# Performance work log

Measured on AMD Instinct MI355X. Metric: run time of the kernel, lower is better.

The kernel has to match this reference:

```python
import jax, jax.numpy as jnp
import numpy as np

B = 262144
MA = [128, 128]
MB = [128, 128]


def krone_linear(x_a, x_b, wa, wb, ba, bb):
    # slice inputs to each branch's in_features (torch slices the wider branch)
    ia, ib = wa.shape[1], wb.shape[1]
    x_a = x_a[:, :ia]
    x_b = x_b[:, :ib]
    h_a = x_a @ wa.T + ba
    h_b = x_b @ wb.T + bb
    # zero-pad the narrower output so both branches share a width (static shapes)
    oa, ob = wa.shape[0], wb.shape[0]
    if oa > ob:
        h_b = jnp.pad(h_b, ((0, 0), (0, oa - ob)))
    elif ob > oa:
        h_a = jnp.pad(h_a, ((0, 0), (0, ob - oa)))
    return h_a, h_b


def krone_softmax(x_a, x_b, fa, fb):
    x_a = x_a[:, :fa]
    x_b = x_b[:, :fb]
    # vectorized per-row Kronecker product: kron(a, b)[i*fb + j] = a[i]*b[j]
    y = (x_a[:, :, None] * x_b[:, None, :]).reshape(x_a.shape[0], fa * fb)
    return jax.nn.softmax(y, axis=1)


def setup_inputs() -> dict:
    key = jax.random.key(0)
    ks = jax.random.split(key, 13)
    s = 0.1
    inp = {
        "x": jax.random.normal(ks[0], (2, B, 2), dtype=jnp.float32),
        "w1a": jax.random.normal(ks[1], (MA[0], 2), dtype=jnp.float32) * s,
        "w1b": jax.random.normal(ks[2], (MB[0], 2), dtype=jnp.float32) * s,
        "b1a": jax.random.normal(ks[3], (MA[0],), dtype=jnp.float32) * s,
        "b1b": jax.random.normal(ks[4], (MB[0],), dtype=jnp.float32) * s,
        "w2a": jax.random.normal(ks[5], (MA[1], MA[0]), dtype=jnp.float32) * s,
        "w2b": jax.random.normal(ks[6], (MB[1], MB[0]), dtype=jnp.float32) * s,
        "b2a": jax.random.normal(ks[7], (MA[1],), dtype=jnp.float32) * s,
        "b2b": jax.random.normal(ks[8], (MB[1],), dtype=jnp.float32) * s,
        "w3a": jax.random.normal(ks[9], (1, MA[1]), dtype=jnp.float32) * s,
        "w3b": jax.random.normal(ks[10], (3, MB[1]), dtype=jnp.float32) * s,
        "b3a": jax.random.normal(ks[11], (1,), dtype=jnp.float32) * s,
        "b3b": jax.random.normal(ks[12], (3,), dtype=jnp.float32) * s,
    }
    return inp


def reference(x, w1a, w1b, b1a, b1b, w2a, w2b, b2a, b2b, w3a, w3b, b3a, b3b):
    x_a, x_b = x[0], x[1]
    h_a, h_b = krone_linear(x_a, x_b, w1a, w1b, b1a, b1b)
    h_a, h_b = jax.nn.relu(h_a), jax.nn.relu(h_b)
    h_a, h_b = krone_linear(h_a, h_b, w2a, w2b, b2a, b2b)
    h_a, h_b = jax.nn.relu(h_a), jax.nn.relu(h_b)
    h_a, h_b = krone_linear(h_a, h_b, w3a, w3b, b3a, b3b)
    return krone_softmax(h_a, h_b, 1, 3)
```

## Files before the change

### kernel.cpp

```cpp
#include <hip/hip_runtime.h>
#include <hip/hip_bf16.h>


#define BTOT 262144
#define NBLK (BTOT / 512)

typedef __attribute__((ext_vector_type(4))) float floatx4;
typedef __attribute__((ext_vector_type(8))) short bf16x8;
typedef __attribute__((ext_vector_type(4))) int  intx4;

#define OFF_W2    0
#define OFF_W1FA  32768
#define OFF_W1FB  40960
#define OFF_B2A   49152
#define OFF_B2B   49664
#define OFF_W3A   50176
#define OFF_W3T   50688
#define OFF_SA    52736
#define LDS_TOTAL 54784

static __device__ __forceinline__ int pack2bf(float lo, float hi) {
    int r;
    asm("v_cvt_pk_bf16_f32 %0, %1, %2" : "=v"(r) : "v"(lo), "v"(hi));
    return r;
}

template <int CTRL>
static __device__ __forceinline__ float dppadd(float v) {
    int t = __builtin_amdgcn_update_dpp(0, __builtin_bit_cast(int, v),
                                        CTRL, 0xF, 0xF, true);
    return v + __builtin_bit_cast(float, t);
}

static __device__ __forceinline__ float red4(float a0, float a1, float a2,
                                             float a3, int col) {
    float s0 = dppadd<0xB1>(a0), s1 = dppadd<0xB1>(a1);
    float s2 = dppadd<0xB1>(a2), s3 = dppadd<0xB1>(a3);
    float u0 = (col & 1) ? s1 : s0;
    float u1 = (col & 1) ? s3 : s2;
    float v0 = dppadd<0x4E>(u0), v1 = dppadd<0x4E>(u1);
    float w  = (col & 2) ? v1 : v0;
    w = dppadd<0x124>(w);
    w = dppadd<0x128>(w);
    return w;
}

static __device__ __forceinline__ void pack_w2(
        unsigned char* dst, int tid, const float* __restrict__ w2) {
    const float4* w2p = (const float4*)w2;
    #pragma unroll
    for (int i = 0; i < 8; ++i) {
        int n  = (tid & 15) | (i << 4);
        int k4 = tid >> 4;
        float4 f = w2p[n * 32 + k4];
        int k = k4 * 4;
        int s = k >> 5;
        int j0 = k & 7;
        int l = ((k & 31) >> 3) * 16 + (n & 15);
        int2 pkd;
        pkd.x = pack2bf(f.x, f.y);
        pkd.y = pack2bf(f.z, f.w);
        *(int2*)(dst + (s * 8 + (n >> 4)) * 1024 + l * 16 + j0 * 2) = pkd;
    }
}

static __device__ __forceinline__ void stage_w1f(
        unsigned char* smem, int off, int tid,
        const float* __restrict__ w1, const float* __restrict__ b1) {
    int tp = tid >> 6, l = tid & 63;
    intx4 e = (intx4){0, 0, 0, 0};
    if (l < 16) {
        int n1 = (tp >> 1) * 32 + (l >> 2) * 8 + (tp & 1) * 4 + (l & 3);
        float w0 = w1[2 * n1], w1v = w1[2 * n1 + 1], bb = b1[n1];
        int dhi = pack2bf(w0, w1v);
        float w0r = __builtin_bit_cast(float, dhi << 16);
        float w1r = __builtin_bit_cast(float, dhi & 0xffff0000);
        int dlo = pack2bf(w0 - w0r, w1v - w1r);
        int bh  = pack2bf(bb, 0.f);
        float bbr = __builtin_bit_cast(float, bh << 16);
        int dbias = pack2bf(bb, bb - bbr);
        e = (intx4){dhi, dlo, dhi, dbias};
    }
    ((intx4*)(smem + off))[tid] = e;
}

static __device__ __forceinline__ intx4 make_xfrag(float2 xx) {
    int d0 = pack2bf(xx.x, xx.y);
    float r0 = __builtin_bit_cast(float, d0 << 16);
    float r1 = __builtin_bit_cast(float, d0 & 0xffff0000);
    int d2 = pack2bf(xx.x - r0, xx.y - r1);
    return (intx4){d0, d0, d2, 0x3f803f80};
}

#define LAYER1_ALL(af, XF, W1Fp)                                               \
    {                                                                          \
        const floatx4 zf = (floatx4){0.f, 0.f, 0.f, 0.f};                      \
        _Pragma("unroll")                                                      \
        for (int s = 0; s < 4; ++s) {                                          \
            bf16x8 a0 = (W1Fp)[(2 * s) * 64 + lane];                           \
            bf16x8 a1 = (W1Fp)[(2 * s + 1) * 64 + lane];                       \
            _Pragma("unroll")                                                  \
            for (int mt = 0; mt < 2; ++mt) {                                   \
                floatx4 td0 = __builtin_amdgcn_mfma_f32_16x16x32_bf16(         \
                    a0, __builtin_bit_cast(bf16x8, (XF)[mt]), zf, 0, 0, 0);    \
                floatx4 td1 = __builtin_amdgcn_mfma_f32_16x16x32_bf16(         \
                    a1, __builtin_bit_cast(bf16x8, (XF)[mt]), zf, 0, 0, 0);    \
                af[s][mt][0] = pack2bf(fmaxf(td0[0], 0.f), fmaxf(td0[1], 0.f));\
                af[s][mt][1] = pack2bf(fmaxf(td0[2], 0.f), fmaxf(td0[3], 0.f));\
                af[s][mt][2] = pack2bf(fmaxf(td1[0], 0.f), fmaxf(td1[1], 0.f));\
                af[s][mt][3] = pack2bf(fmaxf(td1[2], 0.f), fmaxf(td1[3], 0.f));\
            }                                                                  \
        }                                                                      \
    }

#define TTILE(acc0, acc1, af, W2p, B2p, t)                                     \
    floatx4 acc0, acc1;                                                        \
    {                                                                          \
        float b2n = (B2p)[(t) * 16 + col];                                     \
        acc0 = (floatx4){b2n, b2n, b2n, b2n};                                  \
        acc1 = acc0;                                                           \
        _Pragma("unroll")                                                      \
        for (int s = 0; s < 4; ++s) {                                          \
            bf16x8 bfr = (W2p)[(s * 8 + (t)) * 64 + lane];                     \
            acc0 = __builtin_amdgcn_mfma_f32_16x16x32_bf16(                    \
                __builtin_bit_cast(bf16x8, af[s][0]), bfr, acc0, 0, 0, 0);     \
            acc1 = __builtin_amdgcn_mfma_f32_16x16x32_bf16(                    \
                __builtin_bit_cast(bf16x8, af[s][1]), bfr, acc1, 0, 0, 0);     \
        }                                                                      \
    }

__global__ __launch_bounds__(512, 4)
void krone_fused(const float* __restrict__ x,
                 const float* __restrict__ w1a, const float* __restrict__ w1b,
                 const float* __restrict__ b1a, const float* __restrict__ b1b,
                 const float* __restrict__ w2a, const float* __restrict__ w2b,
                 const float* __restrict__ b2a, const float* __restrict__ b2b,
                 const float* __restrict__ w3a, const float* __restrict__ w3b,
                 const float* __restrict__ b3a, const float* __restrict__ b3b,
                 float* __restrict__ out) {
    __shared__ __align__(16) unsigned char smem[LDS_TOTAL];

    const int tid  = threadIdx.x;
    const int lane = tid & 63;
    const int wave = tid >> 6;
    const int quad = lane >> 4;
    const int col  = lane & 15;
    const int wbase = blockIdx.x * 512 + wave * 64;

    const bf16x8* W2   = (const bf16x8*)(smem + OFF_W2);
    const bf16x8* W1FA = (const bf16x8*)(smem + OFF_W1FA);
    const bf16x8* W1FB = (const bf16x8*)(smem + OFF_W1FB);
    const float*  B2A  = (const float*)(smem + OFF_B2A);
    const float*  B2B  = (const float*)(smem + OFF_B2B);
    const float*  W3A  = (const float*)(smem + OFF_W3A);
    const floatx4* W3T = (const floatx4*)(smem + OFF_W3T);
    float*        SA   = (float*)(smem + OFF_SA);
    const float2* xA = (const float2*)x;
    const float2* xB = xA + BTOT;

    const float b3a_ = b3a[0];
    const float b30 = b3b[0], b31 = b3b[1], b32 = b3b[2];

    float2 xv[4];
    #pragma unroll
    for (int c = 0; c < 2; ++c)
        #pragma unroll
        for (int mt = 0; mt < 2; ++mt)
            xv[c * 2 + mt] = xA[wbase + c * 32 + mt * 16 + col];

    pack_w2(smem + OFF_W2, tid, w2a);
    stage_w1f(smem, OFF_W1FA, tid, w1a, b1a);
    stage_w1f(smem, OFF_W1FB, tid, w1b, b1b);
    if (tid < 128) {
        ((float*)(smem + OFF_B2A))[tid] = b2a[tid];
        ((float*)(smem + OFF_B2B))[tid] = b2b[tid];
        ((float*)(smem + OFF_W3A))[tid] = w3a[tid];
    }
    if (tid < 384) {
        int j = tid >> 7, n = tid & 127;
        ((float*)(smem + OFF_W3T))[n * 4 + j] = w3b[tid];
    }
    __syncthreads();

    #pragma unroll
    for (int c = 0; c < 2; ++c) {
        intx4 xf[2];
        #pragma unroll
        for (int mt = 0; mt < 2; ++mt) xf[mt] = make_xfrag(xv[c * 2 + mt]);
        intx4 af[4][2];
        LAYER1_ALL(af, xf, W1FA);

        float pa[2][4] = {};
        #pragma unroll
        for (int t = 0; t < 8; ++t) {
            float w3n = W3A[t * 16 + col];
            TTILE(acc0, acc1, af, W2, B2A, t);
            #pragma unroll
            for (int r = 0; r < 4; ++r) {
                pa[0][r] = fmaf(w3n, fmaxf(acc0[r], 0.f), pa[0][r]);
                pa[1][r] = fmaf(w3n, fmaxf(acc1[r], 0.f), pa[1][r]);
            }
        }
        #pragma unroll
        for (int mt = 0; mt < 2; ++mt) {
            float w = red4(pa[mt][0], pa[mt][1], pa[mt][2], pa[mt][3], col);
            if (col < 4) {
                int sl = mt * 16 + quad * 4 + col;
                SA[wave * 64 + c * 32 + sl] = (w + b3a_) * 1.44269504089f;
            }
        }
    }

    #pragma unroll
    for (int c = 0; c < 2; ++c)
        #pragma unroll
        for (int mt = 0; mt < 2; ++mt)
            xv[c * 2 + mt] = xB[wbase + c * 32 + mt * 16 + col];

    __syncthreads();
    pack_w2(smem + OFF_W2, tid, w2b);
    __syncthreads();

    #pragma unroll
    for (int c = 0; c < 2; ++c) {
        intx4 xf[2];
        #pragma unroll
        for (int mt = 0; mt < 2; ++mt) xf[mt] = make_xfrag(xv[c * 2 + mt]);
        intx4 af[4][2];
        LAYER1_ALL(af, xf, W1FB);

        float p0[2][4] = {}, p1[2][4] = {}, p2[2][4] = {};
        #pragma unroll
        for (int t = 0; t < 8; ++t) {
            floatx4 w3v = W3T[t * 16 + col];
            TTILE(acc0, acc1, af, W2, B2B, t);
            #pragma unroll
            for (int r = 0; r < 4; ++r) {
                float h0 = fmaxf(acc0[r], 0.f);
                float h1 = fmaxf(acc1[r], 0.f);
                p0[0][r] = fmaf(w3v.x, h0, p0[0][r]);
                p1[0][r] = fmaf(w3v.y, h0, p1[0][r]);
                p2[0][r] = fmaf(w3v.z, h0, p2[0][r]);
                p0[1][r] = fmaf(w3v.x, h1, p0[1][r]);
                p1[1][r] = fmaf(w3v.y, h1, p1[1][r]);
                p2[1][r] = fmaf(w3v.z, h1, p2[1][r]);
            }
        }
        #pragma unroll
        for (int mt = 0; mt < 2; ++mt) {
            float t0 = red4(p0[mt][0], p0[mt][1], p0[mt][2], p0[mt][3], col) + b30;
            float t1 = red4(p1[mt][0], p1[mt][1], p1[mt][2], p1[mt][3], col) + b31;
            float t2 = red4(p2[mt][0], p2[mt][1], p2[mt][2], p2[mt][3], col) + b32;
            if (col < 4) {
                int sl = mt * 16 + quad * 4 + col;
                float sa = SA[wave * 64 + c * 32 + sl];
                float y0 = sa * t0, y1 = sa * t1, y2 = sa * t2;
                float m = fmaxf(y0, fmaxf(y1, y2));
                float e0 = exp2f(y0 - m), e1 = exp2f(y1 - m), e2 = exp2f(y2 - m);
                float rs = __builtin_amdgcn_rcpf(e0 + e1 + e2);
                long o = (long)(wbase + c * 32 + sl) * 3;
                out[o]     = e0 * rs;
                out[o + 1] = e1 * rs;
                out[o + 2] = e2 * rs;
            }
        }
    }
}

extern "C" void kernel_launch(void* const* d_in, const int* in_sizes, int n_in,
                              void* d_out, int out_size, void* d_ws, size_t ws_size,
                              hipStream_t stream) {
    const float* x   = (const float*)d_in[0];
    const float* w1a = (const float*)d_in[1];
    const float* w1b = (const float*)d_in[2];
    const float* b1a = (const float*)d_in[3];
    const float* b1b = (const float*)d_in[4];
    const float* w2a = (const float*)d_in[5];
    const float* w2b = (const float*)d_in[6];
    const float* b2a = (const float*)d_in[7];
    const float* b2b = (const float*)d_in[8];
    const float* w3a = (const float*)d_in[9];
    const float* w3b = (const float*)d_in[10];
    const float* b3a = (const float*)d_in[11];
    const float* b3b = (const float*)d_in[12];
    float* out = (float*)d_out;

    krone_fused<<<NBLK, 512, 0, stream>>>(x, w1a, w1b, b1a, b1b, w2a, w2b,
                                          b2a, b2b, w3a, w3b, b3a, b3b, out);
}
```

Before: 107.4 us.

## Process all four row tiles at once to reuse W2 fragments; prefetch w2b early

Replaces the two-chunk loop with a single pass over four 16-row M tiles, so each W2 fragment read from LDS feeds four MFMAs instead of two. The w2b weights are loaded into registers at kernel start and packed into LDS later, hiding that global load latency behind branch A's compute. The larger accumulator and activation arrays raise register pressure, so launch bounds drop from 4 to 2 blocks per CU, which lowers occupancy.

Measured after the change: 112.1 us. 1.04x slower.

```diff
diff --git a/kernel.cpp b/kernel.cpp
--- a/kernel.cpp
+++ b/kernel.cpp
@@ -45,6 +45,20 @@
     return w;
 }
 
+static __device__ __forceinline__ void w2_store(
+        unsigned char* dst, int tid, int i, float4 f) {
+    int n  = (tid & 15) | (i << 4);
+    int k4 = tid >> 4;
+    int k = k4 * 4;
+    int s = k >> 5;
+    int j0 = k & 7;
+    int l = ((k & 31) >> 3) * 16 + (n & 15);
+    int2 pkd;
+    pkd.x = pack2bf(f.x, f.y);
+    pkd.y = pack2bf(f.z, f.w);
+    *(int2*)(dst + (s * 8 + (n >> 4)) * 1024 + l * 16 + j0 * 2) = pkd;
+}
+
 static __device__ __forceinline__ void pack_w2(
         unsigned char* dst, int tid, const float* __restrict__ w2) {
     const float4* w2p = (const float4*)w2;
@@ -52,15 +66,7 @@
     for (int i = 0; i < 8; ++i) {
         int n  = (tid & 15) | (i << 4);
         int k4 = tid >> 4;
-        float4 f = w2p[n * 32 + k4];
-        int k = k4 * 4;
-        int s = k >> 5;
-        int j0 = k & 7;
-        int l = ((k & 31) >> 3) * 16 + (n & 15);
-        int2 pkd;
-        pkd.x = pack2bf(f.x, f.y);
-        pkd.y = pack2bf(f.z, f.w);
-        *(int2*)(dst + (s * 8 + (n >> 4)) * 1024 + l * 16 + j0 * 2) = pkd;
+        w2_store(dst, tid, i, w2p[n * 32 + k4]);
     }
 }
 
@@ -92,7 +98,7 @@
     return (intx4){d0, d0, d2, 0x3f803f80};
 }
 
-#define LAYER1_ALL(af, XF, W1Fp)                                               \
+#define LAYER1_ALL_M(af, XF, W1Fp)                                             \
     {                                                                          \
         const floatx4 zf = (floatx4){0.f, 0.f, 0.f, 0.f};                      \
         _Pragma("unroll")                                                      \
@@ -100,36 +106,36 @@
             bf16x8 a0 = (W1Fp)[(2 * s) * 64 + lane];                           \
             bf16x8 a1 = (W1Fp)[(2 * s + 1) * 64 + lane];                       \
             _Pragma("unroll")                                                  \
-            for (int mt = 0; mt < 2; ++mt) {                                   \
+            for (int m = 0; m < 4; ++m) {                                      \
                 floatx4 td0 = __builtin_amdgcn_mfma_f32_16x16x32_bf16(         \
-                    a0, __builtin_bit_cast(bf16x8, (XF)[mt]), zf, 0, 0, 0);    \
+                    a0, __builtin_bit_cast(bf16x8, (XF)[m]), zf, 0, 0, 0);     \
                 floatx4 td1 = __builtin_amdgcn_mfma_f32_16x16x32_bf16(         \
-                    a1, __builtin_bit_cast(bf16x8, (XF)[mt]), zf, 0, 0, 0);    \
-                af[s][mt][0] = pack2bf(fmaxf(td0[0], 0.f), fmaxf(td0[1], 0.f));\
-                af[s][mt][1] = pack2bf(fmaxf(td0[2], 0.f), fmaxf(td0[3], 0.f));\
-                af[s][mt][2] = pack2bf(fmaxf(td1[0], 0.f), fmaxf(td1[1], 0.f));\
-                af[s][mt][3] = pack2bf(fmaxf(td1[2], 0.f), fmaxf(td1[3], 0.f));\
+                    a1, __builtin_bit_cast(bf16x8, (XF)[m]), zf, 0, 0, 0);     \
+                af[s][m][0] = pack2bf(fmaxf(td0[0], 0.f), fmaxf(td0[1], 0.f)); \
+                af[s][m][1] = pack2bf(fmaxf(td0[2], 0.f), fmaxf(td0[3], 0.f)); \
+                af[s][m][2] = pack2bf(fmaxf(td1[0], 0.f), fmaxf(td1[1], 0.f)); \
+                af[s][m][3] = pack2bf(fmaxf(td1[2], 0.f), fmaxf(td1[3], 0.f)); \
             }                                                                  \
         }                                                                      \
     }
 
-#define TTILE(acc0, acc1, af, W2p, B2p, t)                                     \
-    floatx4 acc0, acc1;                                                        \
+#define TTILE_M(acc, af, W2p, b2n, t)                                          \
+    floatx4 acc[4];                                                            \
     {                                                                          \
-        float b2n = (B2p)[(t) * 16 + col];                                     \
-        acc0 = (floatx4){b2n, b2n, b2n, b2n};                                  \
-        acc1 = acc0;                                                           \
+        _Pragma("unroll")                                                      \
+        for (int m = 0; m < 4; ++m) acc[m] = (floatx4){b2n, b2n, b2n, b2n};    \
         _Pragma("unroll")                                                      \
         for (int s = 0; s < 4; ++s) {                                          \
             bf16x8 bfr = (W2p)[(s * 8 + (t)) * 64 + lane];                     \
-            acc0 = __builtin_amdgcn_mfma_f32_16x16x32_bf16(                    \
-                __builtin_bit_cast(bf16x8, af[s][0]), bfr, acc0, 0, 0, 0);     \
-            acc1 = __builtin_amdgcn_mfma_f32_16x16x32_bf16(                    \
-                __builtin_bit_cast(bf16x8, af[s][1]), bfr, acc1, 0, 0, 0);     \
+            _Pragma("unroll")                                                  \
+            for (int m = 0; m < 4; ++m)                                        \
+                acc[m] = __builtin_amdgcn_mfma_f32_16x16x32_bf16(              \
+                    __builtin_bit_cast(bf16x8, af[s][m]), bfr, acc[m],         \
+                    0, 0, 0);                                                  \
         }                                                                      \
     }
 
-__global__ __launch_bounds__(512, 4)
+__global__ __launch_bounds__(512, 2)
 void krone_fused(const float* __restrict__ x,
                  const float* __restrict__ w1a, const float* __restrict__ w1b,
                  const float* __restrict__ b1a, const float* __restrict__ b1b,
@@ -163,10 +169,18 @@
 
     float2 xv[4];
     #pragma unroll
-    for (int c = 0; c < 2; ++c)
-        #pragma unroll
-        for (int mt = 0; mt < 2; ++mt)
-            xv[c * 2 + mt] = xA[wbase + c * 32 + mt * 16 + col];
+    for (int m = 0; m < 4; ++m) xv[m] = xA[wbase + m * 16 + col];
+
+    float4 wb[8];
+    {
+        const float4* w2bp = (const float4*)w2b;
+        #pragma unroll
+        for (int i = 0; i < 8; ++i) {
+            int n  = (tid & 15) | (i << 4);
+            int k4 = tid >> 4;
+            wb[i] = w2bp[n * 32 + k4];
+        }
+    }
 
     pack_w2(smem + OFF_W2, tid, w2a);
     stage_w1f(smem, OFF_W1FA, tid, w1a, b1a);
@@ -182,83 +196,80 @@
     }
     __syncthreads();
 
-    #pragma unroll
-    for (int c = 0; c < 2; ++c) {
-        intx4 xf[2];
-        #pragma unroll
-        for (int mt = 0; mt < 2; ++mt) xf[mt] = make_xfrag(xv[c * 2 + mt]);
-        intx4 af[4][2];
-        LAYER1_ALL(af, xf, W1FA);
-
-        float pa[2][4] = {};
+    {
+        intx4 xf[4];
+        #pragma unroll
+        for (int m = 0; m < 4; ++m) xf[m] = make_xfrag(xv[m]);
+        intx4 af[4][4];
+        LAYER1_ALL_M(af, xf, W1FA);
+
+        float pa[4][4] = {};
         #pragma unroll
         for (int t = 0; t < 8; ++t) {
             float w3n = W3A[t * 16 + col];
-            TTILE(acc0, acc1, af, W2, B2A, t);
+            float b2n = B2A[t * 16 + col];
+            TTILE_M(acc, af, W2, b2n, t);
             #pragma unroll
-            for (int r = 0; r < 4; ++r) {
-                pa[0][r] = fmaf(w3n, fmaxf(acc0[r], 0.f), pa[0][r]);
-                pa[1][r] = fmaf(w3n, fmaxf(acc1[r], 0.f), pa[1][r]);
-            }
-        }
-        #pragma unroll
-        for (int mt = 0; mt < 2; ++mt) {
-            float w = red4(pa[mt][0], pa[mt][1], pa[mt][2], pa[mt][3], col);
-            if (col < 4) {
-                int sl = mt * 16 + quad * 4 + col;
-                SA[wave * 64 + c * 32 + sl] = (w + b3a_) * 1.44269504089f;
-            }
+            for (int m = 0; m < 4; ++m)
+                #pragma unroll
+                for (int r = 0; r < 4; ++r)
+                    pa[m][r] = fmaf(w3n, fmaxf(acc[m][r], 0.f), pa[m][r]);
+        }
+        #pragma unroll
+        for (int m = 0; m < 4; ++m) {
+            float w = red4(pa[m][0], pa[m][1], pa[m][2], pa[m][3], col);
+            if (col < 4)
+                SA[wave * 64 + m * 16 + quad * 4 + col] =
+                    (w + b3a_) * 1.44269504089f;
         }
     }
 
     #pragma unroll
-    for (int c = 0; c < 2; ++c)
-        #pragma unroll
-        for (int mt = 0; mt < 2; ++mt)
-            xv[c * 2 + mt] = xB[wbase + c * 32 + mt * 16 + col];
+    for (int m = 0; m < 4; ++m) xv[m] = xB[wbase + m * 16 + col];
 
     __syncthreads();
-    pack_w2(smem + OFF_W2, tid, w2b);
+    #pragma unroll
+    for (int i = 0; i < 8; ++i)
+        w2_store((unsigned char*)(smem + OFF_W2), tid, i, wb[i]);
     __syncthreads();
 
-    #pragma unroll
-    for (int c = 0; c < 2; ++c) {
-        intx4 xf[2];
-        #pragma unroll
-        for (int mt = 0; mt < 2; ++mt) xf[mt] = make_xfrag(xv[c * 2 + mt]);
-        intx4 af[4][2];
-        LAYER1_ALL(af, xf, W1FB);
-
-        float p0[2][4] = {}, p1[2][4] = {}, p2[2][4] = {};
+    {
+        intx4 xf[4];
+        #pragma unroll
+        for (int m = 0; m < 4; ++m) xf[m] = make_xfrag(xv[m]);
+        intx4 af[4][4];
+        LAYER1_ALL_M(af, xf, W1FB);
+
+        float p0[4][4] = {}, p1[4][4] = {}, p2[4][4] = {};
         #pragma unroll
         for (int t = 0; t < 8; ++t) {
             floatx4 w3v = W3T[t * 16 + col];
-            TTILE(acc0, acc1, af, W2, B2B, t);
+            float b2n = B2B[t * 16 + col];
+            TTILE_M(acc, af, W2, b2n, t);
             #pragma unroll
-            for (int r = 0; r < 4; ++r) {
-                float h0 = fmaxf(acc0[r], 0.f);
-                float h1 = fmaxf(acc1[r], 0.f);
-                p0[0][r] = fmaf(w3v.x, h0, p0[0][r]);
-                p1[0][r] = fmaf(w3v.y, h0, p1[0][r]);
-                p2[0][r] = fmaf(w3v.z, h0, p2[0][r]);
-                p0[1][r] = fmaf(w3v.x, h1, p0[1][r]);
-                p1[1][r] = fmaf(w3v.y, h1, p1[1][r]);
-                p2[1][r] = fmaf(w3v.z, h1, p2[1][r]);
-            }
-        }
-        #pragma unroll
-        for (int mt = 0; mt < 2; ++mt) {
-            float t0 = red4(p0[mt][0], p0[mt][1], p0[mt][2], p0[mt][3], col) + b30;
-            float t1 = red4(p1[mt][0], p1[mt][1], p1[mt][2], p1[mt][3], col) + b31;
-            float t2 = red4(p2[mt][0], p2[mt][1], p2[mt][2], p2[mt][3], col) + b32;
+            for (int m = 0; m < 4; ++m)
+                #pragma unroll
+                for (int r = 0; r < 4; ++r) {
+                    float h = fmaxf(acc[m][r], 0.f);
+                    p0[m][r] = fmaf(w3v.x, h, p0[m][r]);
+                    p1[m][r] = fmaf(w3v.y, h, p1[m][r]);
+                    p2[m][r] = fmaf(w3v.z, h, p2[m][r]);
+                }
+        }
+        #pragma unroll
+        for (int m = 0; m < 4; ++m) {
+            float t0 = red4(p0[m][0], p0[m][1], p0[m][2], p0[m][3], col) + b30;
+            float t1 = red4(p1[m][0], p1[m][1], p1[m][2], p1[m][3], col) + b31;
+            float t2 = red4(p2[m][0], p2[m][1], p2[m][2], p2[m][3], col) + b32;
             if (col < 4) {
-                int sl = mt * 16 + quad * 4 + col;
-                float sa = SA[wave * 64 + c * 32 + sl];
+                int sl = m * 16 + quad * 4 + col;
+                float sa = SA[wave * 64 + sl];
                 float y0 = sa * t0, y1 = sa * t1, y2 = sa * t2;
-                float m = fmaxf(y0, fmaxf(y1, y2));
-                float e0 = exp2f(y0 - m), e1 = exp2f(y1 - m), e2 = exp2f(y2 - m);
+                float mx = fmaxf(y0, fmaxf(y1, y2));
+                float e0 = exp2f(y0 - mx), e1 = exp2f(y1 - mx),
+                      e2 = exp2f(y2 - mx);
                 float rs = __builtin_amdgcn_rcpf(e0 + e1 + e2);
-                long o = (long)(wbase + c * 32 + sl) * 3;
+                long o = (long)(wbase + sl) * 3;
                 out[o]     = e0 * rs;
                 out[o + 1] = e1 * rs;
                 out[o + 2] = e2 * rs;
```
